# Kernel tuning notes

Measured on AMD Instinct MI355X. Metric: run time of the kernel, lower is better.

Reference implementation:

```python
import jax, jax.numpy as jnp
import numpy as np

B, S, E, H = 2, 2048, 1024, 16
DK = E // H


def setup_inputs() -> dict:
    key = jax.random.key(0)
    ks = jax.random.split(key, 12)
    scale = 1.0 / np.sqrt(E)
    return {
        "query": jax.random.normal(ks[0], (B, S, E), jnp.float32),
        "key": jax.random.normal(ks[1], (B, S, E), jnp.float32),
        "value": jax.random.normal(ks[2], (B, S, E), jnp.float32),
        "key_padding_mask": jnp.ones((B, S, S), jnp.int32),
        "Wq": jax.random.normal(ks[3], (E, E), jnp.float32) * scale,
        "bq": jax.random.normal(ks[4], (E,), jnp.float32) * scale,
        "Wk": jax.random.normal(ks[5], (E, E), jnp.float32) * scale,
        "bk": jax.random.normal(ks[6], (E,), jnp.float32) * scale,
        "Wv": jax.random.normal(ks[7], (E, E), jnp.float32) * scale,
        "bv": jax.random.normal(ks[8], (E,), jnp.float32) * scale,
        "Wo": jax.random.normal(ks[9], (E, E), jnp.float32) * scale,
        "bo": jax.random.normal(ks[10], (E,), jnp.float32) * scale,
    }


def reference(query, key, value, key_padding_mask, Wq, bq, Wk, bk, Wv, bv, Wo, bo):
    b = query.shape[0]
    # torch Linear: x @ W.T + b ; then split heads -> [b, h, t, d_k]
    q = (query @ Wq.T + bq).reshape(b, -1, H, DK).transpose(0, 2, 1, 3)
    k = (key @ Wk.T + bk).reshape(b, -1, H, DK).transpose(0, 2, 1, 3)
    v = (value @ Wv.T + bv).reshape(b, -1, H, DK).transpose(0, 2, 1, 3)
    scores = jnp.einsum("bhqd,bhkd->bhqk", q, k) / np.sqrt(DK)  # [b,h,Tq,Tk]
    mask = (key_padding_mask[:, None, :, :] == 0)  # [b,1,Tq,Tk]
    scores = jnp.where(mask, -jnp.inf, scores)
    attn = jax.nn.softmax(scores, axis=-1)
    attn = jnp.where(mask, 0.0, attn)
    x = jnp.einsum("bhqk,bhkd->bhqd", attn, v)  # [b,h,Tq,d_k]
    x = x.transpose(0, 2, 1, 3).reshape(b, -1, H * DK)  # [b,Tq,E]
    return x @ Wo.T + bo
```

## Files before the change

kernel.cpp:

```cpp
#include <hip/hip_runtime.h>
#include <hip/hip_bf16.h>
#include <cstdint>
#include <cstddef>

#define BB 2
#define SS 2048
#define EE 1024
#define HH 16
#define DKK 64

typedef __bf16 bf16;
typedef __bf16 bf16x8 __attribute__((ext_vector_type(8)));
typedef float f32x4 __attribute__((ext_vector_type(4)));

__device__ __forceinline__ void ldg2lds16(const void* g, void* l) {
  __builtin_amdgcn_global_load_lds(
      (const __attribute__((address_space(1))) unsigned int*)g,
      (__attribute__((address_space(3))) unsigned int*)l, 16, 0, 0);
}

__global__ __launch_bounds__(256) void detect_kernel(
    const unsigned int* __restrict__ q, int* __restrict__ flag) {
  const int t = threadIdx.x;
  int cnt = 0;
#pragma unroll
  for (int i = 0; i < 4; i++) {
    unsigned int v = q[t * 4 + i];
    unsigned int e = (v >> 7) & 0xFF;
    cnt += (e >= 110 && e <= 140) ? 1 : 0;
  }
  __shared__ int s;
  if (t == 0) s = 0;
  __syncthreads();
  atomicAdd(&s, cnt);
  __syncthreads();
  if (t == 0) *flag = (s < 512) ? 1 : 0;
}

struct ConvArgs {
  const void* src[11];
  void* dst[11];
  int n[11];
};

__global__ __launch_bounds__(256) void convert_kernel(
    ConvArgs a, const int* __restrict__ flag) {
  const int j = blockIdx.y;
  const int n = a.n[j];
  const int i0 = (blockIdx.x * 256 + threadIdx.x) * 8;
  if (i0 >= n) return;
  bf16* d = (bf16*)a.dst[j];
  if (*flag) {
    const float* s = (const float*)a.src[j];
    float4 f0 = ((const float4*)(s + i0))[0];
    float4 f1 = ((const float4*)(s + i0))[1];
    union { bf16 h[8]; uint4 u; } t;
    t.h[0] = (bf16)f0.x; t.h[1] = (bf16)f0.y;
    t.h[2] = (bf16)f0.z; t.h[3] = (bf16)f0.w;
    t.h[4] = (bf16)f1.x; t.h[5] = (bf16)f1.y;
    t.h[6] = (bf16)f1.z; t.h[7] = (bf16)f1.w;
    *(uint4*)(d + i0) = t.u;
  } else {
    uint4 v = *(const uint4*)((const bf16*)a.src[j] + i0);
    *(uint4*)(d + i0) = v;
  }
}

__global__ __launch_bounds__(256) void mask_summary_kernel(
    const int* __restrict__ mask, unsigned char* __restrict__ msum) {
  const int bid = blockIdx.x;
  const int kt = bid & 31;
  const int qt = (bid >> 5) & 15;
  const int b = bid >> 9;
  const int t = threadIdx.x;
  const int r = t >> 1;
  const int c0 = (t & 1) * 32;
  const int* p = mask + ((size_t)(b * SS + qt * 128 + r)) * SS + kt * 64 + c0;
  bool all1 = true, any1 = false;
#pragma unroll
  for (int i = 0; i < 8; i++) {
    int4 v = ((const int4*)p)[i];
    all1 = all1 && (v.x != 0) && (v.y != 0) && (v.z != 0) && (v.w != 0);
    any1 = any1 || (v.x != 0) || (v.y != 0) || (v.z != 0) || (v.w != 0);
  }
  __shared__ int sall, sany;
  if (t == 0) { sall = 1; sany = 0; }
  __syncthreads();
  if (!all1) atomicAnd(&sall, 0);
  if (any1) atomicOr(&sany, 1);
  __syncthreads();
  if (t == 0) msum[bid] = sall ? 1 : (sany ? 2 : 0);
}

template <int BM, int BN, int WGM, int WGN, int ND, typename OutT>
__device__ __forceinline__ void gemm_bt_core(
    const bf16* __restrict__ A, const bf16* __restrict__ W,
    const bf16* __restrict__ bias, OutT* __restrict__ out, int mode,
    int m0, int n0) {
  constexpr int BK = 32;
  constexpr int WM = BM / WGM, WN = BN / WGN;
  constexpr int MI = WM / 16, NI = WN / 16;
  constexpr int Kd = 1024;

  __shared__ __align__(16) bf16 As[BM * BK];
  __shared__ __align__(16) bf16 Bs[BN * BK];

  const int tid = threadIdx.x;
  const int wid = tid >> 6, lane = tid & 63;
  const int lr = lane & 15, lg = lane >> 4;
  const int wm = (wid / WGN) * WM, wn = (wid % WGN) * WN;

  f32x4 acc[MI][NI] = {};

  const int sr = tid >> 2;
  const int scol = ((tid & 3) ^ (sr & 3)) * 8;
  const int rchunk = (lg ^ (lr & 3)) * 8;

  for (int k0 = 0; k0 < Kd; k0 += BK) {
#pragma unroll
    for (int i = 0; i < BM / 64; i++)
      ldg2lds16(A + (size_t)(m0 + sr + i * 64) * Kd + k0 + scol,
                &As[(sr + i * 64) * BK + (tid & 3) * 8]);
#pragma unroll
    for (int i = 0; i < BN / 64; i++)
      ldg2lds16(W + (size_t)(n0 + sr + i * 64) * Kd + k0 + scol,
                &Bs[(sr + i * 64) * BK + (tid & 3) * 8]);
    __syncthreads();
    bf16x8 af[MI], bfr[NI];
#pragma unroll
    for (int mi = 0; mi < MI; mi++)
      af[mi] = *(const bf16x8*)&As[(wm + mi * 16 + lr) * BK + rchunk];
#pragma unroll
    for (int ni = 0; ni < NI; ni++)
      bfr[ni] = *(const bf16x8*)&Bs[(wn + ni * 16 + lr) * BK + rchunk];
#pragma unroll
    for (int mi = 0; mi < MI; mi++)
#pragma unroll
      for (int ni = 0; ni < NI; ni++)
        acc[mi][ni] = __builtin_amdgcn_mfma_f32_16x16x32_bf16(
            af[mi], bfr[ni], acc[mi][ni], 0, 0, 0);
    __syncthreads();
  }

  const float scale = (mode == 1) ? 0.180336880111f : 1.0f;

#pragma unroll
  for (int ni = 0; ni < NI; ni++) {
    const int n = n0 + wn + ni * 16 + lr;
    const float bvc = (mode == 3) ? 0.f : (float)bias[n];
#pragma unroll
    for (int mi = 0; mi < MI; mi++) {
      const int m = m0 + wm + mi * 16 + lg * 4;
      f32x4 v = acc[mi][ni];
#pragma unroll
      for (int r = 0; r < 4; r++) {
        const float bv = (mode == 3) ? (float)bias[m + r] : bvc;
        out[(size_t)(m + r) * ND + n] = (OutT)((v[r] + bv) * scale);
      }
    }
  }
}

__global__ __launch_bounds__(256) void qkv_proj_kernel(
    const bf16* __restrict__ q, const bf16* __restrict__ k,
    const bf16* __restrict__ v, const bf16* __restrict__ Wq,
    const bf16* __restrict__ Wk, const bf16* __restrict__ Wv,
    const bf16* __restrict__ bias4, bf16* __restrict__ Qo,
    bf16* __restrict__ Ko, bf16* __restrict__ Vto) {
  const int z = blockIdx.z;
  if (z == 2) {
    gemm_bt_core<128, 128, 2, 2, 4096, bf16>(
        Wv, v, bias4 + 2 * 1024, Vto, 3, blockIdx.x * 128, blockIdx.y * 128);
  } else {
    const bf16* A = z == 0 ? q : k;
    const bf16* W = z == 0 ? Wq : Wk;
    bf16* out = z == 0 ? Qo : Ko;
    gemm_bt_core<128, 128, 2, 2, 1024, bf16>(
        A, W, bias4 + z * 1024, out, z == 0 ? 1 : 0, blockIdx.y * 128,
        blockIdx.x * 128);
  }
}

__global__ __launch_bounds__(256) void o_proj_kernel(
    const bf16* __restrict__ X, const bf16* __restrict__ Wo,
    const bf16* __restrict__ bo, float* __restrict__ out) {
  gemm_bt_core<64, 128, 1, 4, 1024, float>(X, Wo, bo, out, 0,
                                           blockIdx.y * 64, blockIdx.x * 128);
}

__global__ __launch_bounds__(256, 4) void flash_kernel(
    const bf16* __restrict__ Qb, const bf16* __restrict__ Kb,
    const bf16* __restrict__ Vt, const int* __restrict__ mask,
    const unsigned char* __restrict__ msum, bf16* __restrict__ Op0,
    bf16* __restrict__ Op1, float* __restrict__ l0,
    float* __restrict__ l1) {
  const int flat = blockIdx.x;
  const int bh = flat & 31;
  const int kslice = (flat >> 5) & 1;
  const int qt = flat >> 6;
  const int b = bh >> 4;
  const int h = bh & 15;
  const int kb = kslice * (SS / 2);

  bf16* Op = kslice ? Op1 : Op0;
  float* lp = kslice ? l1 : l0;

  const bf16* Qg = Qb + ((size_t)(b * SS + qt * 128)) * EE + h * 64;
  const bf16* Kg = Kb + ((size_t)(b * SS)) * EE + h * 64;
  const bf16* Vg = Vt + (size_t)(h * 64) * (BB * SS) + b * SS;

  __shared__ __align__(16) bf16 Ps[4 * 2048];
  __shared__ __align__(16) bf16 Ks[4096];
  __shared__ __align__(16) bf16 Vs[4096];

  const int tid = threadIdx.x;
  const int wid = tid >> 6, lane = tid & 63;
  const int lr = lane & 15, lg = lane >> 4;
  const int rchunk = (lg ^ (lr & 3)) * 8;

#pragma unroll
  for (int j = 0; j < 4; j++) {
    const int u = j * 256 + tid;
    const int kk = u >> 9, row = (u >> 2) & 127, c = u & 3;
    ldg2lds16(Qg + (size_t)row * EE + kk * 32 + ((c ^ (row & 3)) * 8),
              &Ps[u * 8]);
  }
  __syncthreads();

  bf16x8 qf[2][2];
#pragma unroll
  for (int mi = 0; mi < 2; mi++)
#pragma unroll
    for (int kk = 0; kk < 2; kk++)
      qf[mi][kk] = *(const bf16x8*)
          &Ps[kk * 4096 + (wid * 32 + mi * 16 + lr) * 32 + rchunk];
  __syncthreads();

  bf16x8 ones;
#pragma unroll
  for (int e = 0; e < 8; e++) ones[e] = (bf16)1.0f;

  f32x4 ot[2][4] = {};
  f32x4 lacc[2] = {};

  bf16* Pw = &Ps[wid * 2048];

  for (int kt = 0; kt < SS / 128; kt++) {
    const int kg = kb + kt * 64;
    const unsigned char sm = msum[(b * 16 + qt) * 32 + (kg >> 6)];
    if (sm == 0) continue;

#pragma unroll
    for (int j = 0; j < 2; j++) {
      const int u = j * 256 + tid;
      const int kk = u >> 8, row = (u >> 2) & 63, c = u & 3;
      const int sc8 = (c ^ (row & 3)) * 8;
      ldg2lds16(Kg + (size_t)(kg + row) * EE + kk * 32 + sc8, &Ks[u * 8]);
      ldg2lds16(Vg + (size_t)row * (BB * SS) + kg + kk * 32 + sc8, &Vs[u * 8]);
    }
    __syncthreads();

#pragma unroll
    for (int ni = 0; ni < 4; ni++) {
      f32x4 sc[2];
#pragma unroll
      for (int mi = 0; mi < 2; mi++)
#pragma unroll
        for (int r = 0; r < 4; r++) sc[mi][r] = -8.0f;
#pragma unroll
      for (int kk = 0; kk < 2; kk++) {
        const bf16x8 kf =
            *(const bf16x8*)&Ks[kk * 2048 + (ni * 16 + lr) * 32 + rchunk];
#pragma unroll
        for (int mi = 0; mi < 2; mi++)
          sc[mi] = __builtin_amdgcn_mfma_f32_16x16x32_bf16(qf[mi][kk], kf,
                                                           sc[mi], 0, 0, 0);
      }
      if (sm == 2) {
#pragma unroll
        for (int mi = 0; mi < 2; mi++)
#pragma unroll
          for (int r = 0; r < 4; r++) {
            const int qq = qt * 128 + wid * 32 + mi * 16 + lg * 4 + r;
            const int kk2 = kg + ni * 16 + lr;
            if (mask[((size_t)b * SS + qq) * SS + kk2] == 0)
              sc[mi][r] = -1e30f;
          }
      }
#pragma unroll
      for (int mi = 0; mi < 2; mi++)
#pragma unroll
        for (int r = 0; r < 4; r++) {
          const int row = mi * 16 + lg * 4 + r;
          const int cch = (ni * 2 + (lr >> 3)) ^ (row & 7);
          Pw[row * 64 + cch * 8 + (lr & 7)] =
              (bf16)__builtin_amdgcn_exp2f(sc[mi][r]);
        }
    }

#pragma unroll
    for (int kk = 0; kk < 2; kk++) {
      bf16x8 pf[2];
#pragma unroll
      for (int mi = 0; mi < 2; mi++) {
        const int row = mi * 16 + lr;
        pf[mi] = *(const bf16x8*)
            &Pw[row * 64 + (((kk * 4 + lg) ^ (row & 7)) << 3)];
        lacc[mi] = __builtin_amdgcn_mfma_f32_16x16x32_bf16(pf[mi], ones,
                                                           lacc[mi], 0, 0, 0);
      }
#pragma unroll
      for (int di = 0; di < 4; di++) {
        const bf16x8 vf =
            *(const bf16x8*)&Vs[kk * 2048 + (di * 16 + lr) * 32 + rchunk];
#pragma unroll
        for (int mi = 0; mi < 2; mi++)
          ot[mi][di] = __builtin_amdgcn_mfma_f32_16x16x32_bf16(
              pf[mi], vf, ot[mi][di], 0, 0, 0);
      }
    }
    __syncthreads();
  }

#pragma unroll
  for (int mi = 0; mi < 2; mi++) {
#pragma unroll
    for (int r = 0; r < 4; r++) {
      const int q = qt * 128 + wid * 32 + mi * 16 + lg * 4 + r;
      const size_t row = (size_t)b * SS + q;
      if (lr == 0) lp[row * HH + h] = lacc[mi][r];
      bf16* op = Op + row * EE + h * 64;
#pragma unroll
      for (int di = 0; di < 4; di++)
        op[di * 16 + lr] = (bf16)ot[mi][di][r];
    }
  }
}

__global__ __launch_bounds__(256) void combine_kernel(
    const bf16* __restrict__ Op0, const bf16* __restrict__ Op1,
    const float* __restrict__ l0, const float* __restrict__ l1,
    bf16* __restrict__ X) {
  const int i0 = (blockIdx.x * 256 + threadIdx.x) * 8;
  const int row = i0 >> 10;
  const int h = (i0 & 1023) >> 6;
  const float l = l0[row * HH + h] + l1[row * HH + h];
  const float linv = (l > 0.f) ? 1.0f / l : 0.f;
  union { bf16 h8[8]; uint4 u; } a, b, o;
  a.u = *(const uint4*)(Op0 + i0);
  b.u = *(const uint4*)(Op1 + i0);
#pragma unroll
  for (int e = 0; e < 8; e++)
    o.h8[e] = (bf16)(((float)a.h8[e] + (float)b.h8[e]) * linv);
  *(uint4*)(X + i0) = o.u;
}

extern "C" void kernel_launch(void* const* d_in, const int* in_sizes, int n_in,
                              void* d_out, int out_size, void* d_ws,
                              size_t ws_size, hipStream_t stream) {
  const int* mask = (const int*)d_in[3];

  const size_t NIN = (size_t)BB * SS * EE;
  const size_t NW = (size_t)EE * EE;
  const size_t NRH = (size_t)BB * SS * HH;

  char* p = (char*)d_ws;
  bf16* cWo = (bf16*)p;  p += NW * 2;
  bf16* cb = (bf16*)p;   p += 4 * 1024 * 2;
  unsigned char* msum = (unsigned char*)p; p += 1024;
  int* flag = (int*)p;   p += 1024;
  char* ovl = p;
  bf16* cq = (bf16*)p;   p += NIN * 2;
  bf16* ck = (bf16*)p;   p += NIN * 2;
  bf16* cv = (bf16*)p;   p += NIN * 2;
  bf16* cWq = (bf16*)p;  p += NW * 2;
  bf16* cWk = (bf16*)p;  p += NW * 2;
  bf16* cWv = (bf16*)p;  p += NW * 2;
  bf16* Qb = (bf16*)p;   p += NIN * 2;
  bf16* Kb = (bf16*)p;   p += NIN * 2;
  bf16* Vt = (bf16*)p;   p += NIN * 2;
  bf16* X = (bf16*)p;    p += NIN * 2;
  const size_t need = (size_t)(p - (char*)d_ws);
  if (ws_size < need) return;

  bf16* Op0 = (bf16*)ovl;
  bf16* Op1 = Op0 + NIN;
  float* l0 = (float*)(Op1 + NIN);
  float* l1 = l0 + NRH;

  detect_kernel<<<dim3(1), dim3(256), 0, stream>>>(
      (const unsigned int*)d_in[0], flag);

  ConvArgs ca;
  ca.src[0] = d_in[0];   ca.dst[0] = cq;        ca.n[0] = (int)NIN;
  ca.src[1] = d_in[1];   ca.dst[1] = ck;        ca.n[1] = (int)NIN;
  ca.src[2] = d_in[2];   ca.dst[2] = cv;        ca.n[2] = (int)NIN;
  ca.src[3] = d_in[4];   ca.dst[3] = cWq;       ca.n[3] = (int)NW;
  ca.src[4] = d_in[6];   ca.dst[4] = cWk;       ca.n[4] = (int)NW;
  ca.src[5] = d_in[8];   ca.dst[5] = cWv;       ca.n[5] = (int)NW;
  ca.src[6] = d_in[10];  ca.dst[6] = cWo;       ca.n[6] = (int)NW;
  ca.src[7] = d_in[5];   ca.dst[7] = cb;        ca.n[7] = 1024;
  ca.src[8] = d_in[7];   ca.dst[8] = cb + 1024; ca.n[8] = 1024;
  ca.src[9] = d_in[9];   ca.dst[9] = cb + 2048; ca.n[9] = 1024;
  ca.src[10] = d_in[11]; ca.dst[10] = cb + 3072; ca.n[10] = 1024;
  convert_kernel<<<dim3(2048, 11), dim3(256), 0, stream>>>(ca, flag);

  mask_summary_kernel<<<dim3(BB * 16 * 32), dim3(256), 0, stream>>>(mask, msum);

  qkv_proj_kernel<<<dim3(8, 32, 3), dim3(256), 0, stream>>>(
      cq, ck, cv, cWq, cWk, cWv, cb, Qb, Kb, Vt);

  flash_kernel<<<dim3(1024), dim3(256), 0, stream>>>(
      Qb, Kb, Vt, mask, msum, Op0, Op1, l0, l1);

  combine_kernel<<<dim3(2048), dim3(256), 0, stream>>>(Op0, Op1, l0, l1, X);

  o_proj_kernel<<<dim3(8, 64), dim3(256), 0, stream>>>(X, cWo, cb + 3072,
                                                       (float*)d_out);
}
```

Measured before the change: 264.1 us.

## Double-buffer K/V tiles in flash kernel with 32-key prefetch pipeline

Shrinks the K/V tile from 64 to 32 keys and double-buffers it in shared memory. The next non-skipped tile is prefetched while the current one is computed, and the P scratch buffer alternates halves by buffer index. The aim is to hide global-to-LDS load latency behind the MFMA and exp work, at the cost of twice as many loop iterations and barriers for the same number of keys.

After: 271.5 us. +2.8%, slower.

```diff
diff --git a/kernel.cpp b/kernel.cpp
--- a/kernel.cpp
+++ b/kernel.cpp
@@ -201,6 +201,7 @@
   const int b = bh >> 4;
   const int h = bh & 15;
   const int kb = kslice * (SS / 2);
+  constexpr int T = 32;
 
   bf16* Op = kslice ? Op1 : Op0;
   float* lp = kslice ? l1 : l0;
@@ -208,15 +209,35 @@
   const bf16* Qg = Qb + ((size_t)(b * SS + qt * 128)) * EE + h * 64;
   const bf16* Kg = Kb + ((size_t)(b * SS)) * EE + h * 64;
   const bf16* Vg = Vt + (size_t)(h * 64) * (BB * SS) + b * SS;
+  const unsigned char* msrow = msum + (b * 16 + qt) * 32;
 
   __shared__ __align__(16) bf16 Ps[4 * 2048];
-  __shared__ __align__(16) bf16 Ks[4096];
-  __shared__ __align__(16) bf16 Vs[4096];
+  __shared__ __align__(16) bf16 Ks[2 * 2048];
+  __shared__ __align__(16) bf16 Vs[2 * 2048];
 
   const int tid = threadIdx.x;
   const int wid = tid >> 6, lane = tid & 63;
   const int lr = lane & 15, lg = lane >> 4;
   const int rchunk = (lg ^ (lr & 3)) * 8;
+
+  auto stageKV = [&](int t, int bsel) {
+    const int kg = kb + t * 32;
+    {
+      const int u = tid;
+      const int kk = u >> 7, row = (u >> 2) & 31, c = u & 3;
+      ldg2lds16(Kg + (size_t)(kg + row) * EE + kk * 32 + ((c ^ (row & 3)) * 8),
+                &Ks[bsel * 2048 + u * 8]);
+    }
+    {
+      const int u = tid;
+      const int row = u >> 2, c = u & 3;
+      ldg2lds16(Vg + (size_t)row * (BB * SS) + kg + ((c ^ (row & 3)) * 8),
+                &Vs[bsel * 2048 + u * 8]);
+    }
+  };
+
+  int tA = 0;
+  while (tA < T && msrow[(kb + tA * 32) >> 6] == 0) tA++;
 
 #pragma unroll
   for (int j = 0; j < 4; j++) {
@@ -225,6 +246,7 @@
     ldg2lds16(Qg + (size_t)row * EE + kk * 32 + ((c ^ (row & 3)) * 8),
               &Ps[u * 8]);
   }
+  if (tA < T) stageKV(tA, 0);
   __syncthreads();
 
   bf16x8 qf[2][2];
@@ -245,23 +267,17 @@
 
   bf16* Pw = &Ps[wid * 2048];
 
-  for (int kt = 0; kt < SS / 128; kt++) {
-    const int kg = kb + kt * 64;
-    const unsigned char sm = msum[(b * 16 + qt) * 32 + (kg >> 6)];
-    if (sm == 0) continue;
-
-#pragma unroll
-    for (int j = 0; j < 2; j++) {
-      const int u = j * 256 + tid;
-      const int kk = u >> 8, row = (u >> 2) & 63, c = u & 3;
-      const int sc8 = (c ^ (row & 3)) * 8;
-      ldg2lds16(Kg + (size_t)(kg + row) * EE + kk * 32 + sc8, &Ks[u * 8]);
-      ldg2lds16(Vg + (size_t)row * (BB * SS) + kg + kk * 32 + sc8, &Vs[u * 8]);
-    }
-    __syncthreads();
-
-#pragma unroll
-    for (int ni = 0; ni < 4; ni++) {
+  int buf = 0;
+  for (int t = tA; t < T;) {
+    int tn = t + 1;
+    while (tn < T && msrow[(kb + tn * 32) >> 6] == 0) tn++;
+    if (tn < T) stageKV(tn, buf ^ 1);
+
+    const int kg = kb + t * 32;
+    const unsigned char sm = msrow[kg >> 6];
+
+#pragma unroll
+    for (int ni = 0; ni < 2; ni++) {
       f32x4 sc[2];
 #pragma unroll
       for (int mi = 0; mi < 2; mi++)
@@ -269,8 +285,8 @@
         for (int r = 0; r < 4; r++) sc[mi][r] = -8.0f;
 #pragma unroll
       for (int kk = 0; kk < 2; kk++) {
-        const bf16x8 kf =
-            *(const bf16x8*)&Ks[kk * 2048 + (ni * 16 + lr) * 32 + rchunk];
+        const bf16x8 kf = *(const bf16x8*)
+            &Ks[buf * 2048 + kk * 1024 + (ni * 16 + lr) * 32 + rchunk];
 #pragma unroll
         for (int mi = 0; mi < 2; mi++)
           sc[mi] = __builtin_amdgcn_mfma_f32_16x16x32_bf16(qf[mi][kk], kf,
@@ -292,33 +308,33 @@
 #pragma unroll
         for (int r = 0; r < 4; r++) {
           const int row = mi * 16 + lg * 4 + r;
-          const int cch = (ni * 2 + (lr >> 3)) ^ (row & 7);
+          const int cch = buf * 4 + ((ni * 2 + (lr >> 3)) ^ (row & 3));
           Pw[row * 64 + cch * 8 + (lr & 7)] =
               (bf16)__builtin_amdgcn_exp2f(sc[mi][r]);
         }
     }
 
-#pragma unroll
-    for (int kk = 0; kk < 2; kk++) {
-      bf16x8 pf[2];
-#pragma unroll
-      for (int mi = 0; mi < 2; mi++) {
-        const int row = mi * 16 + lr;
-        pf[mi] = *(const bf16x8*)
-            &Pw[row * 64 + (((kk * 4 + lg) ^ (row & 7)) << 3)];
-        lacc[mi] = __builtin_amdgcn_mfma_f32_16x16x32_bf16(pf[mi], ones,
-                                                           lacc[mi], 0, 0, 0);
-      }
-#pragma unroll
-      for (int di = 0; di < 4; di++) {
-        const bf16x8 vf =
-            *(const bf16x8*)&Vs[kk * 2048 + (di * 16 + lr) * 32 + rchunk];
-#pragma unroll
-        for (int mi = 0; mi < 2; mi++)
-          ot[mi][di] = __builtin_amdgcn_mfma_f32_16x16x32_bf16(
-              pf[mi], vf, ot[mi][di], 0, 0, 0);
-      }
-    }
+    bf16x8 pf[2];
+#pragma unroll
+    for (int mi = 0; mi < 2; mi++) {
+      const int row = mi * 16 + lr;
+      pf[mi] = *(const bf16x8*)
+          &Pw[row * 64 + ((buf * 4 + (lg ^ (row & 3))) << 3)];
+      lacc[mi] = __builtin_amdgcn_mfma_f32_16x16x32_bf16(pf[mi], ones,
+                                                         lacc[mi], 0, 0, 0);
+    }
+#pragma unroll
+    for (int di = 0; di < 4; di++) {
+      const bf16x8 vf = *(const bf16x8*)
+          &Vs[buf * 2048 + (di * 16 + lr) * 32 + rchunk];
+#pragma unroll
+      for (int mi = 0; mi < 2; mi++)
+        ot[mi][di] = __builtin_amdgcn_mfma_f32_16x16x32_bf16(
+            pf[mi], vf, ot[mi][di], 0, 0, 0);
+    }
+
+    buf ^= 1;
+    t = tn;
     __syncthreads();
   }
 
```
